# Performance work log

Measured on AMD Instinct MI355X. Metric: run time of the kernel, lower is better.

The kernel has to match this reference:

```python
import jax, jax.numpy as jnp
import numpy as np

B, N, M = 256, 2048, 64          # batch, memory locations, memory width
C, R, WH, SR = 512, 4, 4, 1      # controller dim, read heads, write heads, shift radius
DE, DO = 256, 256                # external input dim, NTM output dim
SHIFT = 2 * SR + 1
PR = M + 3 + SHIFT               # key + beta + gate + shift + gamma
PW = PR + 2 * M                  # + erase + add
EPS = 1e-8


def setup_inputs() -> dict:
    key = jax.random.key(0)
    ks = jax.random.split(key, 13)
    return {
        "external_input": jax.random.normal(ks[0], (B, DE), jnp.float32),
        "past_readings": jax.random.normal(ks[1], (B, R, M), jnp.float32),
        "past_read_w": jax.nn.softmax(jax.random.normal(ks[2], (R, B, N), jnp.float32), axis=-1),
        "past_write_w": jax.nn.softmax(jax.random.normal(ks[3], (WH, B, N), jnp.float32), axis=-1),
        "memory": jax.random.normal(ks[4], (B, N, M), jnp.float32),
        "ctrl_W": jax.random.normal(ks[5], (DE + R * M, C), jnp.float32) * 0.02,
        "ctrl_b": jnp.zeros((C,), jnp.float32),
        "read_W": jax.random.normal(ks[6], (R, C, PR), jnp.float32) * 0.02,
        "read_b": jnp.zeros((R, PR), jnp.float32),
        "write_W": jax.random.normal(ks[7], (WH, C, PW), jnp.float32) * 0.02,
        "write_b": jnp.zeros((WH, PW), jnp.float32),
        "out_W": jax.random.normal(ks[8], (C + R * M, DO), jnp.float32) * 0.02,
        "out_b": jnp.zeros((DO,), jnp.float32),
    }


def _address(p, memory, w_prev):
    """Standard NTM addressing. p: [B, >=PR], memory: [B,N,M], w_prev: [B,N]."""
    k = p[:, :M]                                              # content key
    beta = jax.nn.softplus(p[:, M:M + 1])                     # key strength
    g = jax.nn.sigmoid(p[:, M + 1:M + 2])                     # interpolation gate
    s = jax.nn.softmax(p[:, M + 2:M + 2 + SHIFT], axis=-1)    # shift weights
    gamma = 1.0 + jax.nn.softplus(p[:, M + 2 + SHIFT:M + 3 + SHIFT])  # sharpening
    mem_norm = jnp.linalg.norm(memory, axis=-1)               # [B,N]
    k_norm = jnp.linalg.norm(k, axis=-1, keepdims=True)       # [B,1]
    cos = jnp.einsum('bnm,bm->bn', memory, k) / (mem_norm * k_norm + EPS)
    w_c = jax.nn.softmax(beta * cos, axis=-1)                 # content addressing
    w_g = g * w_c + (1.0 - g) * w_prev                        # interpolation
    # circular shift convolution (small fixed window)
    w_s = sum(s[:, off + SR:off + SR + 1] * jnp.roll(w_g, off, axis=-1)
              for off in range(-SR, SR + 1))
    w_pow = (w_s + EPS) ** gamma                              # sharpening
    return w_pow / jnp.sum(w_pow, axis=-1, keepdims=True)


def reference(external_input, past_readings, past_read_w, past_write_w, memory,
              ctrl_W, ctrl_b, read_W, read_b, write_W, write_b, out_W, out_b):
    ctrl_in = jnp.concatenate([external_input, past_readings.reshape(B, -1)], axis=1)
    ctrl = ctrl_in @ ctrl_W + ctrl_b                          # [B,C]
    # --- read heads (vectorized over heads) ---
    rp = jnp.einsum('bc,hcp->hbp', ctrl, read_W) + read_b[:, None, :]
    new_read_w = jax.vmap(_address, in_axes=(0, None, 0))(rp, memory, past_read_w)  # [R,B,N]
    reads = jnp.einsum('hbn,bnm->hbm', new_read_w, memory)    # [R,B,M]
    read_out = jnp.swapaxes(reads, 0, 1).reshape(B, R * M)    # matches concat(axis=1) order
    # --- write heads (sequential: each mutates memory) ---
    new_write_w = []
    for h in range(WH):
        p = ctrl @ write_W[h] + write_b[h]                    # [B,PW]
        w = _address(p[:, :PR], memory, past_write_w[h])      # [B,N]
        erase = jax.nn.sigmoid(p[:, PR:PR + M])               # [B,M]
        add = jnp.tanh(p[:, PR + M:PR + 2 * M])               # [B,M]
        memory = memory * (1.0 - w[:, :, None] * erase[:, None, :]) \
                 + w[:, :, None] * add[:, None, :]
        new_write_w.append(w)
    new_write_w = jnp.stack(new_write_w, axis=0)              # [WH,B,N]
    ntm_out = jnp.concatenate([ctrl, read_out], axis=1) @ out_W + out_b
    return (ntm_out, memory, read_out, new_read_w, new_write_w)
```

## Files before the change

kernel.cpp:

```cpp
#include <hip/hip_runtime.h>
#include <math.h>

#define EPSV 1e-8f

#define O_MEM 65536
#define O_RO  33619968
#define O_NRW 33685504
#define O_NWW 35782656

__device__ __forceinline__ float sp_(float x){ return fmaxf(x,0.f) + log1pf(expf(-fabsf(x))); }
__device__ __forceinline__ float sg_(float x){ return 1.f/(1.f+expf(-x)); }

struct CM { const float* P; int S; float bv; float* dst; };

__device__ __forceinline__ CM cmap(int c, int b,
    const float* __restrict__ rW, const float* __restrict__ rB,
    const float* __restrict__ wW, const float* __restrict__ wB,
    const float* __restrict__ oW,
    float* __restrict__ rp, float* __restrict__ wp, float* __restrict__ out)
{
  CM m;
  if (c < 280){
    int h = c/70, j = c - h*70;
    m.P = rW + (size_t)h*35840 + j;  m.S = 70;
    m.bv = rB[c];
    m.dst = rp + ((size_t)h*256 + b)*70 + j;
  } else if (c < 1072){
    int c2 = c - 280, h = c2/198, j = c2 - h*198;
    m.P = wW + (size_t)h*101376 + j; m.S = 198;
    m.bv = wB[c2];
    m.dst = wp + ((size_t)h*256 + b)*198 + j;
  } else {
    int j = c - 1072;
    m.P = oW + j;                    m.S = 256;
    m.bv = 0.f;
    m.dst = out + (size_t)b*256 + j;
  }
  return m;
}

__global__ __launch_bounds__(512) void k_proj(
    const float* __restrict__ ext, const float* __restrict__ prd,
    const float* __restrict__ cW, const float* __restrict__ cB,
    const float* __restrict__ rW, const float* __restrict__ rB,
    const float* __restrict__ wW, const float* __restrict__ wB,
    const float* __restrict__ oW,
    float* __restrict__ rp, float* __restrict__ wp, float* __restrict__ out)
{
  __shared__ float ins[512];
  __shared__ float cs[512];
  const int t = threadIdx.x, b = blockIdx.x;
  ins[t] = (t < 256) ? ext[(size_t)b*256 + t] : prd[(size_t)b*256 + (t - 256)];
  __syncthreads();

  {
    float a0=0.f, a1=0.f, a2=0.f, a3=0.f;
    const float* W = cW + t;
    #pragma unroll 4
    for (int k=0; k<512; k+=4){
      float4 iv = *(const float4*)&ins[k];
      a0 = fmaf(iv.x, W[(k+0)*512], a0);
      a1 = fmaf(iv.y, W[(k+1)*512], a1);
      a2 = fmaf(iv.z, W[(k+2)*512], a2);
      a3 = fmaf(iv.w, W[(k+3)*512], a3);
    }
    cs[t] = (a0+a1)+(a2+a3) + cB[t];
  }
  __syncthreads();

  {
    CM m0 = cmap(t,       b, rW,rB,wW,wB,oW, rp,wp,out);
    CM m1 = cmap(t + 512, b, rW,rB,wW,wB,oW, rp,wp,out);
    const float* P0 = m0.P; const int S0 = m0.S;
    const float* P1 = m1.P; const int S1 = m1.S;
    float a00=0.f,a01=0.f,a02=0.f,a03=0.f;
    float a10=0.f,a11=0.f,a12=0.f,a13=0.f;
    #pragma unroll 4
    for (int k=0; k<512; k+=4){
      float4 cv = *(const float4*)&cs[k];
      a00 = fmaf(cv.x, P0[(k+0)*S0], a00);
      a10 = fmaf(cv.x, P1[(k+0)*S1], a10);
      a01 = fmaf(cv.y, P0[(k+1)*S0], a01);
      a11 = fmaf(cv.y, P1[(k+1)*S1], a11);
      a02 = fmaf(cv.z, P0[(k+2)*S0], a02);
      a12 = fmaf(cv.z, P1[(k+2)*S1], a12);
      a03 = fmaf(cv.w, P0[(k+3)*S0], a03);
      a13 = fmaf(cv.w, P1[(k+3)*S1], a13);
    }
    *m0.dst = (a00+a01)+(a02+a03) + m0.bv;
    *m1.dst = (a10+a11)+(a12+a13) + m1.bv;

    if (t < 304){
      CM m2 = cmap(t + 1024, b, rW,rB,wW,wB,oW, rp,wp,out);
      const float* P2 = m2.P; const int S2 = m2.S;
      float b0=0.f,b1=0.f,b2=0.f,b3=0.f;
      #pragma unroll 4
      for (int k=0; k<512; k+=4){
        float4 cv = *(const float4*)&cs[k];
        b0 = fmaf(cv.x, P2[(k+0)*S2], b0);
        b1 = fmaf(cv.y, P2[(k+1)*S2], b1);
        b2 = fmaf(cv.z, P2[(k+2)*S2], b2);
        b3 = fmaf(cv.w, P2[(k+3)*S2], b3);
      }
      *m2.dst = (b0+b1)+(b2+b3) + m2.bv;
    }
  }
}


__device__ __forceinline__ float blockMax(float v, float* red){
  #pragma unroll
  for (int o=32;o;o>>=1) v = fmaxf(v, __shfl_down(v,o,64));
  __syncthreads();
  if ((threadIdx.x & 63) == 0) red[threadIdx.x>>6] = v;
  __syncthreads();
  float m = red[0];
  #pragma unroll
  for (int i=1;i<8;i++) m = fmaxf(m, red[i]);
  return m;
}
__device__ __forceinline__ float blockSum(float v, float* red){
  #pragma unroll
  for (int o=32;o;o>>=1) v += __shfl_down(v,o,64);
  __syncthreads();
  if ((threadIdx.x & 63) == 0) red[threadIdx.x>>6] = v;
  __syncthreads();
  float s = red[0];
  #pragma unroll
  for (int i=1;i<8;i++) s += red[i];
  return s;
}

__device__ void addressing(float* c, const float* __restrict__ wprev, float* __restrict__ wout,
                           float beta, float g, float s0, float s1, float s2, float gam,
                           float* red, int t){
  int base = t*4;
  float lv[4];
  {
    float4 cv = *(const float4*)&c[base];
    lv[0]=beta*cv.x; lv[1]=beta*cv.y; lv[2]=beta*cv.z; lv[3]=beta*cv.w;
  }
  float mx = fmaxf(fmaxf(lv[0],lv[1]), fmaxf(lv[2],lv[3]));
  mx = blockMax(mx, red);
  float sm = 0.f;
  #pragma unroll
  for (int i=0;i<4;i++){ lv[i] = expf(lv[i]-mx); sm += lv[i]; }
  sm = blockSum(sm, red);
  float inv = 1.f/sm;
  float gi = 1.f - g;
  {
    float4 wp4 = *(const float4*)&wprev[base];
    lv[0] = g*lv[0]*inv + gi*wp4.x;
    lv[1] = g*lv[1]*inv + gi*wp4.y;
    lv[2] = g*lv[2]*inv + gi*wp4.z;
    lv[3] = g*lv[3]*inv + gi*wp4.w;
  }
  *(float4*)&c[base] = make_float4(lv[0],lv[1],lv[2],lv[3]);
  __syncthreads();
  float left  = c[(base+2047)&2047];
  float right = c[(base+4)&2047];
  __syncthreads();
  float pw[4]; float ps=0.f;
  #pragma unroll
  for (int i=0;i<4;i++){
    float wm1 = (i==0)? left  : lv[i-1];
    float wp1 = (i==3)? right : lv[i+1];
    float wsv = s0*wp1 + s1*lv[i] + s2*wm1;
    float p = expf(gam * logf(wsv + EPSV));
    pw[i]=p; ps+=p;
  }
  ps = blockSum(ps, red);
  float invp = 1.f/ps;
  float4 wo = make_float4(pw[0]*invp, pw[1]*invp, pw[2]*invp, pw[3]*invp);
  *(float4*)&c[base] = wo;
  *(float4*)&wout[base] = wo;
  __syncthreads();
}

template<int NUPD, int NCOS, int KS0>
__device__ __forceinline__ void cos_pass(const float* __restrict__ gmb,
    float (*slots)[2048], const float* __restrict__ kr, const float* __restrict__ kw,
    const float* __restrict__ er, const float* __restrict__ aw,
    const float* __restrict__ kn, int t)
{
  const int row0 = t>>2, q = t&3, cb = q<<4;
  float4 kk[NCOS][4];
  float knl[NCOS];
  #pragma unroll
  for (int c=0;c<NCOS;c++){
    const int ks = (NCOS==5)? c : KS0;
    const float* kb = (ks<4)? (kr + ks*64) : (kw + (ks-4)*64);
    #pragma unroll
    for (int j=0;j<4;j++) kk[c][j] = *(const float4*)&kb[cb + 4*j];
    knl[c] = kn[ks];
  }
  float4 ee[NUPD>0?NUPD:1][4], aa[NUPD>0?NUPD:1][4];
  #pragma unroll
  for (int h=0;h<NUPD;h++){
    #pragma unroll
    for (int j=0;j<4;j++){
      ee[h][j] = *(const float4*)&er[h*64+cb+4*j];
      aa[h][j] = *(const float4*)&aw[h*64+cb+4*j];
    }
  }
  #pragma unroll 4
  for (int it=0; it<16; ++it){
    const int row = (it<<7) + row0;
    const float4* src = (const float4*)(gmb + ((size_t)row<<6) + cb);
    float4 v[4];
    #pragma unroll
    for (int j=0;j<4;j++) v[j] = src[j];
    #pragma unroll
    for (int h=0;h<NUPD;h++){
      float w = slots[4+h][row];
      #pragma unroll
      for (int j=0;j<4;j++){
        v[j].x = fmaf(-w, fmaf(v[j].x, ee[h][j].x, -aa[h][j].x), v[j].x);
        v[j].y = fmaf(-w, fmaf(v[j].y, ee[h][j].y, -aa[h][j].y), v[j].y);
        v[j].z = fmaf(-w, fmaf(v[j].z, ee[h][j].z, -aa[h][j].z), v[j].z);
        v[j].w = fmaf(-w, fmaf(v[j].w, ee[h][j].w, -aa[h][j].w), v[j].w);
      }
    }
    float nrm = 0.f;
    float acc[NCOS];
    #pragma unroll
    for (int c=0;c<NCOS;c++) acc[c]=0.f;
    #pragma unroll
    for (int j=0;j<4;j++){
      nrm = fmaf(v[j].x,v[j].x, fmaf(v[j].y,v[j].y, fmaf(v[j].z,v[j].z, fmaf(v[j].w,v[j].w, nrm))));
      #pragma unroll
      for (int c=0;c<NCOS;c++){
        acc[c] = fmaf(v[j].x,kk[c][j].x, fmaf(v[j].y,kk[c][j].y,
                  fmaf(v[j].z,kk[c][j].z, fmaf(v[j].w,kk[c][j].w, acc[c]))));
      }
    }
    nrm += __shfl_xor(nrm,1); nrm += __shfl_xor(nrm,2);
    #pragma unroll
    for (int c=0;c<NCOS;c++){ acc[c] += __shfl_xor(acc[c],1); acc[c] += __shfl_xor(acc[c],2); }
    float mn = sqrtf(nrm);
    if (NCOS==5){
      float av = acc[0], kv = knl[0];
      #pragma unroll
      for (int c=1;c<4;c++){ if (q==c){ av=acc[c]; kv=knl[c]; } }
      slots[q][row] = av/(mn*kv+EPSV);
      if (q==0) slots[4][row] = acc[4]/(mn*knl[4]+EPSV);
    } else {
      if (q==0) slots[KS0][row] = acc[0]/(mn*knl[0]+EPSV);
    }
  }
}

__device__ __forceinline__ void final_pass(const float* __restrict__ gmb,
    float (*slots)[2048], const float* __restrict__ er, const float* __restrict__ aw,
    float4 racc[4][2], float* __restrict__ gout, int t)
{
  const int row0 = t>>3, q = t&7, cb = q<<3;
  float4 ee[4][2], aa[4][2];
  #pragma unroll
  for (int h=0;h<4;h++){
    #pragma unroll
    for (int j=0;j<2;j++){
      ee[h][j] = *(const float4*)&er[h*64+cb+4*j];
      aa[h][j] = *(const float4*)&aw[h*64+cb+4*j];
    }
  }
  #pragma unroll 4
  for (int it=0; it<32; ++it){
    const int row = (it<<6) + row0;
    const float4* src = (const float4*)(gmb + ((size_t)row<<6) + cb);
    float4 v0 = src[0], v1 = src[1];
    #pragma unroll
    for (int h=0;h<4;h++){
      float wr = slots[h][row];
      racc[h][0].x = fmaf(wr, v0.x, racc[h][0].x);
      racc[h][0].y = fmaf(wr, v0.y, racc[h][0].y);
      racc[h][0].z = fmaf(wr, v0.z, racc[h][0].z);
      racc[h][0].w = fmaf(wr, v0.w, racc[h][0].w);
      racc[h][1].x = fmaf(wr, v1.x, racc[h][1].x);
      racc[h][1].y = fmaf(wr, v1.y, racc[h][1].y);
      racc[h][1].z = fmaf(wr, v1.z, racc[h][1].z);
      racc[h][1].w = fmaf(wr, v1.w, racc[h][1].w);
    }
    #pragma unroll
    for (int h=0;h<4;h++){
      float w = slots[4+h][row];
      v0.x = fmaf(-w, fmaf(v0.x, ee[h][0].x, -aa[h][0].x), v0.x);
      v0.y = fmaf(-w, fmaf(v0.y, ee[h][0].y, -aa[h][0].y), v0.y);
      v0.z = fmaf(-w, fmaf(v0.z, ee[h][0].z, -aa[h][0].z), v0.z);
      v0.w = fmaf(-w, fmaf(v0.w, ee[h][0].w, -aa[h][0].w), v0.w);
      v1.x = fmaf(-w, fmaf(v1.x, ee[h][1].x, -aa[h][1].x), v1.x);
      v1.y = fmaf(-w, fmaf(v1.y, ee[h][1].y, -aa[h][1].y), v1.y);
      v1.z = fmaf(-w, fmaf(v1.z, ee[h][1].z, -aa[h][1].z), v1.z);
      v1.w = fmaf(-w, fmaf(v1.w, ee[h][1].w, -aa[h][1].w), v1.w);
    }
    float4* dst = (float4*)(gout + ((size_t)row<<6) + cb);
    dst[0]=v0; dst[1]=v1;
  }
}

__global__ __launch_bounds__(512) void mega_kernel(
    const float* __restrict__ mem0, const float* __restrict__ prw, const float* __restrict__ pww,
    const float* __restrict__ rp, const float* __restrict__ wp,
    const float* __restrict__ oW, const float* __restrict__ oB, float* __restrict__ out)
{
  const int b = blockIdx.x, t = threadIdx.x;
  __shared__ float slots[8][2048];
  __shared__ float kr[256], kw[256], er[256], aw[256];
  __shared__ float sBeta[8], sG[8], sGam[8], sKn[8], sS0[8], sS1[8], sS2[8];
  __shared__ float red[8];
  __shared__ float ro[256];

  if (t < 256){
    int h = t>>6, m = t&63;
    kr[t] = rp[((size_t)h*256 + b)*70 + m];
    const float* wph = wp + ((size_t)h*256 + b)*198;
    kw[t] = wph[m];
    er[t] = sg_(wph[70+m]);
    aw[t] = tanhf(wph[134+m]);
    if (t < 8){
      int hh = t & 3;
      const float* p = (t>=4) ? (wp + ((size_t)hh*256+b)*198) : (rp + ((size_t)hh*256+b)*70);
      sBeta[t] = sp_(p[64]);
      sG[t]    = sg_(p[65]);
      float a0=p[66], a1=p[67], a2=p[68];
      float mx = fmaxf(a0, fmaxf(a1,a2));
      float e0=expf(a0-mx), e1=expf(a1-mx), e2=expf(a2-mx);
      float inv = 1.f/(e0+e1+e2);
      sS0[t]=e0*inv; sS1[t]=e1*inv; sS2[t]=e2*inv;
      sGam[t]  = 1.f + sp_(p[69]);
    }
  }
  __syncthreads();
  if (t < 8){
    const float* kv = (t>=4) ? (kw + (t&3)*64) : (kr + (t&3)*64);
    float s=0.f;
    for (int m=0;m<64;m++) s = fmaf(kv[m],kv[m],s);
    sKn[t] = sqrtf(s);
  }
  __syncthreads();

  const float* gmb = mem0 + (size_t)b*131072;

  cos_pass<0,5,0>(gmb, slots, kr,kw,er,aw,sKn, t);
  __syncthreads();
  #pragma unroll 1
  for (int h=0;h<4;h++)
    addressing(slots[h], prw + ((size_t)h*256+b)*2048, out + O_NRW + ((size_t)h*256+b)*2048,
               sBeta[h], sG[h], sS0[h], sS1[h], sS2[h], sGam[h], red, t);
  addressing(slots[4], pww + (size_t)b*2048, out + O_NWW + (size_t)b*2048,
             sBeta[4], sG[4], sS0[4], sS1[4], sS2[4], sGam[4], red, t);

  cos_pass<1,1,5>(gmb, slots, kr,kw,er,aw,sKn, t);
  __syncthreads();
  addressing(slots[5], pww + ((size_t)256+b)*2048, out + O_NWW + ((size_t)256+b)*2048,
             sBeta[5], sG[5], sS0[5], sS1[5], sS2[5], sGam[5], red, t);

  cos_pass<2,1,6>(gmb, slots, kr,kw,er,aw,sKn, t);
  __syncthreads();
  addressing(slots[6], pww + ((size_t)512+b)*2048, out + O_NWW + ((size_t)512+b)*2048,
             sBeta[6], sG[6], sS0[6], sS1[6], sS2[6], sGam[6], red, t);

  cos_pass<3,1,7>(gmb, slots, kr,kw,er,aw,sKn, t);
  __syncthreads();
  addressing(slots[7], pww + ((size_t)768+b)*2048, out + O_NWW + ((size_t)768+b)*2048,
             sBeta[7], sG[7], sS0[7], sS1[7], sS2[7], sGam[7], red, t);

  float4 racc[4][2];
  #pragma unroll
  for (int h=0;h<4;h++){ racc[h][0]=make_float4(0,0,0,0); racc[h][1]=make_float4(0,0,0,0); }
  final_pass(gmb, slots, er, aw, racc, out + O_MEM + (size_t)b*131072, t);
  __syncthreads();

  {
    float* scr = (float*)slots;
    #pragma unroll 1
    for (int h=0;h<4;h++){
      *(float4*)&scr[t*8]   = racc[h][0];
      *(float4*)&scr[t*8+4] = racc[h][1];
      __syncthreads();
      if (t < 64){
        int qq = t>>3, c = t&7;
        float s = 0.f;
        for (int g=0; g<64; ++g) s += scr[(g*8+qq)*8 + c];
        out[O_RO + (size_t)b*256 + h*64 + t] = s;
        ro[h*64 + t] = s;
      }
      __syncthreads();
    }
  }

  {
    const int c = t & 255, kh = t >> 8;
    const float* P  = oW + ((size_t)(512 + kh*128))*256 + c;
    const float* rr = ro + kh*128;
    float a0=0.f,a1=0.f,a2=0.f,a3=0.f;
    #pragma unroll 4
    for (int k=0; k<128; k+=4){
      float4 rv = *(const float4*)&rr[k];
      a0 = fmaf(rv.x, P[(k+0)*256], a0);
      a1 = fmaf(rv.y, P[(k+1)*256], a1);
      a2 = fmaf(rv.z, P[(k+2)*256], a2);
      a3 = fmaf(rv.w, P[(k+3)*256], a3);
    }
    float* scr = (float*)slots;
    scr[t] = (a0+a1)+(a2+a3);
    __syncthreads();
    if (t < 256){
      size_t idx = (size_t)b*256 + t;
      out[idx] = out[idx] + scr[t] + scr[t+256] + oB[t];
    }
  }
}


extern "C" void kernel_launch(void* const* d_in, const int* in_sizes, int n_in,
                              void* d_out, int out_size, void* d_ws, size_t ws_size,
                              hipStream_t stream) {
  (void)in_sizes; (void)n_in; (void)out_size; (void)ws_size;
  const float* ext    = (const float*)d_in[0];
  const float* prd    = (const float*)d_in[1];
  const float* prw    = (const float*)d_in[2];
  const float* pww    = (const float*)d_in[3];
  const float* mem0   = (const float*)d_in[4];
  const float* ctrlW  = (const float*)d_in[5];
  const float* ctrlB  = (const float*)d_in[6];
  const float* readW  = (const float*)d_in[7];
  const float* readB  = (const float*)d_in[8];
  const float* writeW = (const float*)d_in[9];
  const float* writeB = (const float*)d_in[10];
  const float* outW   = (const float*)d_in[11];
  const float* outB   = (const float*)d_in[12];
  float* out = (float*)d_out;
  float* ws  = (float*)d_ws;
  float* rp  = ws;
  float* wp  = rp + 71680;

  k_proj<<<256,512,0,stream>>>(ext, prd, ctrlW, ctrlB, readW, readB, writeW, writeB, outW,
                               rp, wp, out);
  mega_kernel<<<256,512,0,stream>>>(mem0, prw, pww, rp, wp, outW, outB, out);
}
```

Before: 459.6 us.

## Double mega_kernel block size to 1024 threads and use nontemporal stores

Raises the per-batch mega_kernel from 512 to 1024 threads. Addressing, cosine, final-pass and output-projection loops are re-partitioned so each thread handles half as many rows or columns, and reduction buffers are resized to 16 waves. Memory-output and weight stores become nontemporal to avoid cache pollution. This aims to hide the latency of streaming the 512KB per-batch memory with more waves per CU, at the cost of more block-wide synchronisation and register pressure under the 1024-thread launch bound.

```diff
diff --git a/kernel.cpp b/kernel.cpp
--- a/kernel.cpp
+++ b/kernel.cpp
@@ -2,6 +2,9 @@
 #include <math.h>
 
 #define EPSV 1e-8f
+
+typedef float f32x2 __attribute__((ext_vector_type(2)));
+typedef float f32x4 __attribute__((ext_vector_type(4)));
 
 #define O_MEM 65536
 #define O_RO  33619968
@@ -10,6 +13,10 @@
 
 __device__ __forceinline__ float sp_(float x){ return fmaxf(x,0.f) + log1pf(expf(-fabsf(x))); }
 __device__ __forceinline__ float sg_(float x){ return 1.f/(1.f+expf(-x)); }
+
+__device__ __forceinline__ void nt_store4(const float4& v, float* p){
+  __builtin_nontemporal_store(*(const f32x4*)&v, (f32x4*)p);
+}
 
 struct CM { const float* P; int S; float bv; float* dst; };
 
@@ -116,7 +123,7 @@
   __syncthreads();
   float m = red[0];
   #pragma unroll
-  for (int i=1;i<8;i++) m = fmaxf(m, red[i]);
+  for (int i=1;i<16;i++) m = fmaxf(m, red[i]);
   return m;
 }
 __device__ __forceinline__ float blockSum(float v, float* red){
@@ -127,53 +134,43 @@
   __syncthreads();
   float s = red[0];
   #pragma unroll
-  for (int i=1;i<8;i++) s += red[i];
+  for (int i=1;i<16;i++) s += red[i];
   return s;
 }
 
 __device__ void addressing(float* c, const float* __restrict__ wprev, float* __restrict__ wout,
                            float beta, float g, float s0, float s1, float s2, float gam,
                            float* red, int t){
-  int base = t*4;
-  float lv[4];
-  {
-    float4 cv = *(const float4*)&c[base];
-    lv[0]=beta*cv.x; lv[1]=beta*cv.y; lv[2]=beta*cv.z; lv[3]=beta*cv.w;
-  }
-  float mx = fmaxf(fmaxf(lv[0],lv[1]), fmaxf(lv[2],lv[3]));
-  mx = blockMax(mx, red);
-  float sm = 0.f;
-  #pragma unroll
-  for (int i=0;i<4;i++){ lv[i] = expf(lv[i]-mx); sm += lv[i]; }
-  sm = blockSum(sm, red);
+  int base = t*2;
+  float lv0, lv1;
+  {
+    float2 cv = *(const float2*)&c[base];
+    lv0 = beta*cv.x; lv1 = beta*cv.y;
+  }
+  float mx = blockMax(fmaxf(lv0,lv1), red);
+  lv0 = expf(lv0-mx); lv1 = expf(lv1-mx);
+  float sm = blockSum(lv0+lv1, red);
   float inv = 1.f/sm;
   float gi = 1.f - g;
   {
-    float4 wp4 = *(const float4*)&wprev[base];
-    lv[0] = g*lv[0]*inv + gi*wp4.x;
-    lv[1] = g*lv[1]*inv + gi*wp4.y;
-    lv[2] = g*lv[2]*inv + gi*wp4.z;
-    lv[3] = g*lv[3]*inv + gi*wp4.w;
-  }
-  *(float4*)&c[base] = make_float4(lv[0],lv[1],lv[2],lv[3]);
+    f32x2 wp2 = __builtin_nontemporal_load((const f32x2*)&wprev[base]);
+    lv0 = g*lv0*inv + gi*wp2.x;
+    lv1 = g*lv1*inv + gi*wp2.y;
+  }
+  *(float2*)&c[base] = make_float2(lv0, lv1);
   __syncthreads();
   float left  = c[(base+2047)&2047];
-  float right = c[(base+4)&2047];
-  __syncthreads();
-  float pw[4]; float ps=0.f;
-  #pragma unroll
-  for (int i=0;i<4;i++){
-    float wm1 = (i==0)? left  : lv[i-1];
-    float wp1 = (i==3)? right : lv[i+1];
-    float wsv = s0*wp1 + s1*lv[i] + s2*wm1;
-    float p = expf(gam * logf(wsv + EPSV));
-    pw[i]=p; ps+=p;
-  }
-  ps = blockSum(ps, red);
+  float right = c[(base+2)&2047];
+  __syncthreads();
+  float ws0 = s0*lv1   + s1*lv0 + s2*left;
+  float ws1 = s0*right + s1*lv1 + s2*lv0;
+  float pw0 = expf(gam * logf(ws0 + EPSV));
+  float pw1 = expf(gam * logf(ws1 + EPSV));
+  float ps = blockSum(pw0+pw1, red);
   float invp = 1.f/ps;
-  float4 wo = make_float4(pw[0]*invp, pw[1]*invp, pw[2]*invp, pw[3]*invp);
-  *(float4*)&c[base] = wo;
-  *(float4*)&wout[base] = wo;
+  float2 wo = make_float2(pw0*invp, pw1*invp);
+  *(float2*)&c[base] = wo;
+  __builtin_nontemporal_store(*(const f32x2*)&wo, (f32x2*)&wout[base]);
   __syncthreads();
 }
 
@@ -204,8 +201,8 @@
     }
   }
   #pragma unroll 4
-  for (int it=0; it<16; ++it){
-    const int row = (it<<7) + row0;
+  for (int it=0; it<8; ++it){
+    const int row = (it<<8) + row0;
     const float4* src = (const float4*)(gmb + ((size_t)row<<6) + cb);
     float4 v[4];
     #pragma unroll
@@ -243,7 +240,7 @@
       #pragma unroll
       for (int c=1;c<4;c++){ if (q==c){ av=acc[c]; kv=knl[c]; } }
       slots[q][row] = av/(mn*kv+EPSV);
-      if (q==0) slots[4][row] = acc[4]/(mn*knl[4]+EPSV);
+      if (q==0) slots[4][row] = acc[NCOS-1]/(mn*knl[NCOS-1]+EPSV);
     } else {
       if (q==0) slots[KS0][row] = acc[0]/(mn*knl[0]+EPSV);
     }
@@ -265,8 +262,8 @@
     }
   }
   #pragma unroll 4
-  for (int it=0; it<32; ++it){
-    const int row = (it<<6) + row0;
+  for (int it=0; it<16; ++it){
+    const int row = (it<<7) + row0;
     const float4* src = (const float4*)(gmb + ((size_t)row<<6) + cb);
     float4 v0 = src[0], v1 = src[1];
     #pragma unroll
@@ -293,12 +290,13 @@
       v1.z = fmaf(-w, fmaf(v1.z, ee[h][1].z, -aa[h][1].z), v1.z);
       v1.w = fmaf(-w, fmaf(v1.w, ee[h][1].w, -aa[h][1].w), v1.w);
     }
-    float4* dst = (float4*)(gout + ((size_t)row<<6) + cb);
-    dst[0]=v0; dst[1]=v1;
-  }
-}
-
-__global__ __launch_bounds__(512) void mega_kernel(
+    float* dst = gout + ((size_t)row<<6) + cb;
+    nt_store4(v0, dst);
+    nt_store4(v1, dst+4);
+  }
+}
+
+__global__ __launch_bounds__(1024) void mega_kernel(
     const float* __restrict__ mem0, const float* __restrict__ prw, const float* __restrict__ pww,
     const float* __restrict__ rp, const float* __restrict__ wp,
     const float* __restrict__ oW, const float* __restrict__ oB, float* __restrict__ out)
@@ -307,7 +305,7 @@
   __shared__ float slots[8][2048];
   __shared__ float kr[256], kw[256], er[256], aw[256];
   __shared__ float sBeta[8], sG[8], sGam[8], sKn[8], sS0[8], sS1[8], sS2[8];
-  __shared__ float red[8];
+  __shared__ float red[16];
   __shared__ float ro[256];
 
   if (t < 256){
@@ -381,8 +379,8 @@
       if (t < 64){
         int qq = t>>3, c = t&7;
         float s = 0.f;
-        for (int g=0; g<64; ++g) s += scr[(g*8+qq)*8 + c];
-        out[O_RO + (size_t)b*256 + h*64 + t] = s;
+        for (int g=0; g<128; ++g) s += scr[(g*8+qq)*8 + c];
+        __builtin_nontemporal_store(s, &out[O_RO + (size_t)b*256 + h*64 + t]);
         ro[h*64 + t] = s;
       }
       __syncthreads();
@@ -391,11 +389,11 @@
 
   {
     const int c = t & 255, kh = t >> 8;
-    const float* P  = oW + ((size_t)(512 + kh*128))*256 + c;
-    const float* rr = ro + kh*128;
+    const float* P  = oW + ((size_t)(512 + kh*64))*256 + c;
+    const float* rr = ro + kh*64;
     float a0=0.f,a1=0.f,a2=0.f,a3=0.f;
     #pragma unroll 4
-    for (int k=0; k<128; k+=4){
+    for (int k=0; k<64; k+=4){
       float4 rv = *(const float4*)&rr[k];
       a0 = fmaf(rv.x, P[(k+0)*256], a0);
       a1 = fmaf(rv.y, P[(k+1)*256], a1);
@@ -407,7 +405,8 @@
     __syncthreads();
     if (t < 256){
       size_t idx = (size_t)b*256 + t;
-      out[idx] = out[idx] + scr[t] + scr[t+256] + oB[t];
+      float v = out[idx] + scr[t] + scr[t+256] + scr[t+512] + scr[t+768] + oB[t];
+      __builtin_nontemporal_store(v, &out[idx]);
     }
   }
 }
@@ -437,5 +436,5 @@
 
   k_proj<<<256,512,0,stream>>>(ext, prd, ctrlW, ctrlB, readW, readB, writeW, writeB, outW,
                                rp, wp, out);
-  mega_kernel<<<256,512,0,stream>>>(mem0, prw, pww, rp, wp, outW, outB, out);
-}
+  mega_kernel<<<256,1024,0,stream>>>(mem0, prw, pww, rp, wp, outW, outB, out);
+}
```

After: 615.2 us. +33.9%, slower.

## Replace two memory re-read passes with rank-1 algebraic cosine updates

Applied to the files above, without the earlier changes.

Write-head cosine similarity after a rank-1 erase/add update is expressed algebraically from per-row statistics (norm, dot products with the next key, erase/add cross terms). These are gathered during an existing memory pass and stored in a new shared aux buffer. The separate global-memory passes for write heads 1 and 3 are dropped, leaving two full memory reads instead of four before the final pass. The cost is extra FMA and shuffle work per pass, 40KB more shared memory per block, and possible cancellation error in the expanded norm formula, which is clamped at zero.

```diff
diff --git a/kernel.cpp b/kernel.cpp
--- a/kernel.cpp
+++ b/kernel.cpp
@@ -177,76 +177,126 @@
   __syncthreads();
 }
 
-template<int NUPD, int NCOS, int KS0>
-__device__ __forceinline__ void cos_pass(const float* __restrict__ gmb,
-    float (*slots)[2048], const float* __restrict__ kr, const float* __restrict__ kw,
+__device__ __forceinline__ void cosA_pass(const float* __restrict__ gmb,
+    float (*slots)[2048], float (*aux)[2048],
+    const float* __restrict__ kr, const float* __restrict__ kw,
     const float* __restrict__ er, const float* __restrict__ aw,
     const float* __restrict__ kn, int t)
 {
   const int row0 = t>>2, q = t&3, cb = q<<4;
-  float4 kk[NCOS][4];
-  float knl[NCOS];
-  #pragma unroll
-  for (int c=0;c<NCOS;c++){
-    const int ks = (NCOS==5)? c : KS0;
-    const float* kb = (ks<4)? (kr + ks*64) : (kw + (ks-4)*64);
-    #pragma unroll
-    for (int j=0;j<4;j++) kk[c][j] = *(const float4*)&kb[cb + 4*j];
-    knl[c] = kn[ks];
-  }
-  float4 ee[NUPD>0?NUPD:1][4], aa[NUPD>0?NUPD:1][4];
-  #pragma unroll
-  for (int h=0;h<NUPD;h++){
-    #pragma unroll
-    for (int j=0;j<4;j++){
-      ee[h][j] = *(const float4*)&er[h*64+cb+4*j];
-      aa[h][j] = *(const float4*)&aw[h*64+cb+4*j];
-    }
-  }
-  #pragma unroll 4
+  float4 kk[5][4];
+  #pragma unroll
+  for (int c=0;c<4;c++){
+    #pragma unroll
+    for (int j=0;j<4;j++) kk[c][j] = *(const float4*)&kr[c*64+cb+4*j];
+  }
+  #pragma unroll
+  for (int j=0;j<4;j++) kk[4][j] = *(const float4*)&kw[cb+4*j];
+  float4 K1[4], E0[4], A0[4];
+  #pragma unroll
+  for (int j=0;j<4;j++){
+    K1[j] = *(const float4*)&kw[64+cb+4*j];
+    E0[j] = *(const float4*)&er[cb+4*j];
+    A0[j] = *(const float4*)&aw[cb+4*j];
+  }
+  float knl[5];
+  #pragma unroll
+  for (int c=0;c<5;c++) knl[c]=kn[c];
+
+  #pragma unroll 2
   for (int it=0; it<16; ++it){
     const int row = (it<<7) + row0;
     const float4* src = (const float4*)(gmb + ((size_t)row<<6) + cb);
     float4 v[4];
     #pragma unroll
     for (int j=0;j<4;j++) v[j] = src[j];
-    #pragma unroll
-    for (int h=0;h<NUPD;h++){
-      float w = slots[4+h][row];
-      #pragma unroll
-      for (int j=0;j<4;j++){
-        v[j].x = fmaf(-w, fmaf(v[j].x, ee[h][j].x, -aa[h][j].x), v[j].x);
-        v[j].y = fmaf(-w, fmaf(v[j].y, ee[h][j].y, -aa[h][j].y), v[j].y);
-        v[j].z = fmaf(-w, fmaf(v[j].z, ee[h][j].z, -aa[h][j].z), v[j].z);
-        v[j].w = fmaf(-w, fmaf(v[j].w, ee[h][j].w, -aa[h][j].w), v[j].w);
-      }
-    }
-    float nrm = 0.f;
-    float acc[NCOS];
-    #pragma unroll
-    for (int c=0;c<NCOS;c++) acc[c]=0.f;
+    float acc0=0,acc1=0,acc2=0,acc3=0,acc4=0;
+    float S1=0,dA=0,dB=0,S2=0,S3=0,C1=0,C2=0;
     #pragma unroll
     for (int j=0;j<4;j++){
-      nrm = fmaf(v[j].x,v[j].x, fmaf(v[j].y,v[j].y, fmaf(v[j].z,v[j].z, fmaf(v[j].w,v[j].w, nrm))));
-      #pragma unroll
-      for (int c=0;c<NCOS;c++){
-        acc[c] = fmaf(v[j].x,kk[c][j].x, fmaf(v[j].y,kk[c][j].y,
-                  fmaf(v[j].z,kk[c][j].z, fmaf(v[j].w,kk[c][j].w, acc[c]))));
-      }
-    }
-    nrm += __shfl_xor(nrm,1); nrm += __shfl_xor(nrm,2);
-    #pragma unroll
-    for (int c=0;c<NCOS;c++){ acc[c] += __shfl_xor(acc[c],1); acc[c] += __shfl_xor(acc[c],2); }
-    float mn = sqrtf(nrm);
-    if (NCOS==5){
-      float av = acc[0], kv = knl[0];
-      #pragma unroll
-      for (int c=1;c<4;c++){ if (q==c){ av=acc[c]; kv=knl[c]; } }
-      slots[q][row] = av/(mn*kv+EPSV);
-      if (q==0) slots[4][row] = acc[4]/(mn*knl[4]+EPSV);
-    } else {
-      if (q==0) slots[KS0][row] = acc[0]/(mn*knl[0]+EPSV);
-    }
+#define COMP(f) { float m=v[j].f, k1v=K1[j].f, e0v=E0[j].f, a0v=A0[j].f; \
+      float m2=m*m; float p=m*k1v; float q2=m2*e0v; float r=m*a0v; \
+      acc0=fmaf(m,kk[0][j].f,acc0); acc1=fmaf(m,kk[1][j].f,acc1); \
+      acc2=fmaf(m,kk[2][j].f,acc2); acc3=fmaf(m,kk[3][j].f,acc3); \
+      acc4=fmaf(m,kk[4][j].f,acc4); \
+      S1+=m2; dA+=p; dB=fmaf(p,e0v,dB); S2+=q2; S3=fmaf(q2,e0v,S3); \
+      C1+=r; C2=fmaf(r,e0v,C2); }
+      COMP(x) COMP(y) COMP(z) COMP(w)
+#undef COMP
+    }
+#define RED(s) s+=__shfl_xor(s,1); s+=__shfl_xor(s,2);
+    RED(acc0) RED(acc1) RED(acc2) RED(acc3) RED(acc4)
+    RED(S1) RED(dA) RED(dB) RED(S2) RED(S3) RED(C1) RED(C2)
+#undef RED
+    float mn = sqrtf(S1);
+    float av = acc0, kv = knl[0];
+    if (q==1){ av=acc1; kv=knl[1]; }
+    if (q==2){ av=acc2; kv=knl[2]; }
+    if (q==3){ av=acc3; kv=knl[3]; }
+    slots[q][row] = av/(mn*kv+EPSV);
+    if (q==0) slots[4][row] = acc4/(mn*knl[4]+EPSV);
+    if (q==1){ aux[0][row]=S1; aux[1][row]=dA; aux[2][row]=dB; }
+    if (q==2){ aux[3][row]=2.f*(C1-S2); aux[4][row]=S3-2.f*C2; }
+  }
+}
+
+__device__ __forceinline__ void cosB_pass(const float* __restrict__ gmb,
+    float (*slots)[2048], float (*aux)[2048],
+    const float* __restrict__ kw,
+    const float* __restrict__ er, const float* __restrict__ aw,
+    const float* __restrict__ kn, int t)
+{
+  const int row0 = t>>2, q = t&3, cb = q<<4;
+  float4 E0[4],A0[4],E1[4],A1[4],K2[4],K3[4],E2[4],A2[4];
+  #pragma unroll
+  for (int j=0;j<4;j++){
+    E0[j]=*(const float4*)&er[cb+4*j];      A0[j]=*(const float4*)&aw[cb+4*j];
+    E1[j]=*(const float4*)&er[64+cb+4*j];   A1[j]=*(const float4*)&aw[64+cb+4*j];
+    K2[j]=*(const float4*)&kw[128+cb+4*j];  K3[j]=*(const float4*)&kw[192+cb+4*j];
+    E2[j]=*(const float4*)&er[128+cb+4*j];  A2[j]=*(const float4*)&aw[128+cb+4*j];
+  }
+  const float kn6 = kn[6];
+  #pragma unroll 2
+  for (int it=0; it<16; ++it){
+    const int row = (it<<7) + row0;
+    const float4* src = (const float4*)(gmb + ((size_t)row<<6) + cb);
+    float4 v[4];
+    #pragma unroll
+    for (int j=0;j<4;j++) v[j] = src[j];
+    const float w0 = slots[4][row], w1 = slots[5][row];
+    float acc2s=0,S1=0,dA=0,dB=0,S2=0,S3=0,C1=0,C2=0;
+    #pragma unroll
+    for (int j=0;j<4;j++){
+#define COMP(f) { float m=v[j].f; \
+      m = fmaf(-w0, fmaf(m,E0[j].f,-A0[j].f), m); \
+      m = fmaf(-w1, fmaf(m,E1[j].f,-A1[j].f), m); \
+      float e2v=E2[j].f; float m2=m*m; float p=m*K3[j].f; float q2=m2*e2v; float r=m*A2[j].f; \
+      acc2s=fmaf(m,K2[j].f,acc2s); \
+      S1+=m2; dA+=p; dB=fmaf(p,e2v,dB); S2+=q2; S3=fmaf(q2,e2v,S3); \
+      C1+=r; C2=fmaf(r,e2v,C2); }
+      COMP(x) COMP(y) COMP(z) COMP(w)
+#undef COMP
+    }
+#define RED(s) s+=__shfl_xor(s,1); s+=__shfl_xor(s,2);
+    RED(acc2s) RED(S1) RED(dA) RED(dB) RED(S2) RED(S3) RED(C1) RED(C2)
+#undef RED
+    if (q==0) slots[6][row] = acc2s/(sqrtf(S1)*kn6+EPSV);
+    if (q==1){ aux[0][row]=S1; aux[1][row]=dA; aux[2][row]=dB; }
+    if (q==2){ aux[3][row]=2.f*(C1-S2); aux[4][row]=S3-2.f*C2; }
+  }
+}
+
+__device__ __forceinline__ void rank1_cos(float* dst, const float* wSlot,
+    float (*aux)[2048], float K, float A, float knv, int t)
+{
+  #pragma unroll
+  for (int i=0;i<4;i++){
+    const int r = t + 512*i;
+    const float w = wSlot[r];
+    const float d = aux[1][r] + w*(K - aux[2][r]);
+    float N = aux[0][r] + w*aux[3][r] + w*w*(aux[4][r] + A);
+    N = fmaxf(N, 0.f);
+    dst[r] = d/(sqrtf(N)*knv + EPSV);
   }
 }
 
@@ -305,6 +355,7 @@
 {
   const int b = blockIdx.x, t = threadIdx.x;
   __shared__ float slots[8][2048];
+  __shared__ float aux[5][2048];
   __shared__ float kr[256], kw[256], er[256], aw[256];
   __shared__ float sBeta[8], sG[8], sGam[8], sKn[8], sS0[8], sS1[8], sS2[8];
   __shared__ float red[8];
@@ -341,7 +392,7 @@
 
   const float* gmb = mem0 + (size_t)b*131072;
 
-  cos_pass<0,5,0>(gmb, slots, kr,kw,er,aw,sKn, t);
+  cosA_pass(gmb, slots, aux, kr,kw,er,aw,sKn, t);
   __syncthreads();
   #pragma unroll 1
   for (int h=0;h<4;h++)
@@ -350,17 +401,25 @@
   addressing(slots[4], pww + (size_t)b*2048, out + O_NWW + (size_t)b*2048,
              sBeta[4], sG[4], sS0[4], sS1[4], sS2[4], sGam[4], red, t);
 
-  cos_pass<1,1,5>(gmb, slots, kr,kw,er,aw,sKn, t);
+  {
+    float K01=0.f, A00=0.f;
+    for (int m=0;m<64;m++){ float av=aw[m]; K01=fmaf(av,kw[64+m],K01); A00=fmaf(av,av,A00); }
+    rank1_cos(slots[5], slots[4], aux, K01, A00, sKn[5], t);
+  }
   __syncthreads();
   addressing(slots[5], pww + ((size_t)256+b)*2048, out + O_NWW + ((size_t)256+b)*2048,
              sBeta[5], sG[5], sS0[5], sS1[5], sS2[5], sGam[5], red, t);
 
-  cos_pass<2,1,6>(gmb, slots, kr,kw,er,aw,sKn, t);
+  cosB_pass(gmb, slots, aux, kw,er,aw,sKn, t);
   __syncthreads();
   addressing(slots[6], pww + ((size_t)512+b)*2048, out + O_NWW + ((size_t)512+b)*2048,
              sBeta[6], sG[6], sS0[6], sS1[6], sS2[6], sGam[6], red, t);
 
-  cos_pass<3,1,7>(gmb, slots, kr,kw,er,aw,sKn, t);
+  {
+    float K23=0.f, A22=0.f;
+    for (int m=0;m<64;m++){ float av=aw[128+m]; K23=fmaf(av,kw[192+m],K23); A22=fmaf(av,av,A22); }
+    rank1_cos(slots[7], slots[6], aux, K23, A22, sKn[7], t);
+  }
   __syncthreads();
   addressing(slots[7], pww + ((size_t)768+b)*2048, out + O_NWW + ((size_t)768+b)*2048,
              sBeta[7], sG[7], sS0[7], sS1[7], sS2[7], sGam[7], red, t);
```

Measured after the change: 441.3 us. 4.0% less time.
